# Kernel optimization log

Measured on AMD Instinct MI355X. Metric: run time of the kernel, lower is better.

The kernel has to match this reference:

```python
import jax, jax.numpy as jnp
import numpy as np

N = 50000; E = 800000; H = 4; C = 64; FEAT = 128; EDIM = 16; G = 256
NEG_SLOPE = 0.2; BN_EPS = 1e-5


def _gat_layer(x, src, dst, W, a_src, a_dst, bias, gamma, beta, alpha_edge=None):
    # GATConv (concat=True, PyG math), then BatchNorm1d (batch stats) + ReLU.
    h = (x @ W).reshape(N, H, C)                       # [N,H,C]
    alpha = (h * a_src).sum(-1)[src] + (h * a_dst).sum(-1)[dst]   # [Etot,H]
    if alpha_edge is not None:
        alpha = alpha + alpha_edge
    alpha = jax.nn.leaky_relu(alpha, NEG_SLOPE)
    amax = jax.ops.segment_max(alpha, dst, num_segments=N)        # edge softmax over dst
    ea = jnp.exp(alpha - amax[dst])
    denom = jax.ops.segment_sum(ea, dst, num_segments=N)
    coef = ea / (denom[dst] + 1e-16)
    out = jax.ops.segment_sum(coef[:, :, None] * h[src], dst, num_segments=N)
    out = out.reshape(N, H * C) + bias
    mu = out.mean(0)
    var = out.var(0)
    out = (out - mu) / jnp.sqrt(var + BN_EPS) * gamma + beta
    return jax.nn.relu(out)


def setup_inputs() -> dict:
    key = jax.random.key(0)
    ks = jax.random.split(key, 32)
    s = 0.05
    inp = {
        "x": jax.random.normal(ks[0], (N, FEAT), jnp.float32),
        "edge_index": jax.random.randint(ks[1], (2, E), 0, N),
        "edge_attr": jax.random.normal(ks[2], (E, EDIM), jnp.float32),
        "batch": jnp.sort(jax.random.randint(ks[3], (N,), 0, G)),
    }
    in_dims = [FEAT, H * C, H * C]
    for i in range(3):
        k = 4 + 7 * i
        inp[f"W{i}"] = jax.random.normal(ks[k], (in_dims[i], H * C), jnp.float32) * s
        inp[f"att_src{i}"] = jax.random.normal(ks[k + 1], (H, C), jnp.float32) * s
        inp[f"att_dst{i}"] = jax.random.normal(ks[k + 2], (H, C), jnp.float32) * s
        inp[f"bias{i}"] = jnp.zeros((H * C,), jnp.float32)
        inp[f"gamma{i}"] = jnp.ones((H * C,), jnp.float32)
        inp[f"beta{i}"] = jnp.zeros((H * C,), jnp.float32)
    inp["We0"] = jax.random.normal(ks[28], (EDIM, H * C), jnp.float32) * s
    inp["att_e0"] = jax.random.normal(ks[29], (H, C), jnp.float32) * s
    return inp


def reference(x, edge_index, edge_attr, batch,
              W0, att_src0, att_dst0, bias0, gamma0, beta0,
              W1, att_src1, att_dst1, bias1, gamma1, beta1,
              W2, att_src2, att_dst2, bias2, gamma2, beta2,
              We0, att_e0):
    # PyG GATConv adds self-loops; edge_attr for self-loops filled with mean.
    loops = jnp.arange(N)
    src = jnp.concatenate([edge_index[0], loops])
    dst = jnp.concatenate([edge_index[1], loops])
    ea_sl = jnp.concatenate([edge_attr, jnp.broadcast_to(edge_attr.mean(0), (N, EDIM))], 0)
    e = (ea_sl @ We0).reshape(E + N, H, C)
    alpha_e = (e * att_e0).sum(-1)                     # [Etot,H]
    x = _gat_layer(x, src, dst, W0, att_src0, att_dst0, bias0, gamma0, beta0, alpha_e)
    x = _gat_layer(x, src, dst, W1, att_src1, att_dst1, bias1, gamma1, beta1)
    x = _gat_layer(x, src, dst, W2, att_src2, att_dst2, bias2, gamma2, beta2)
    # global_mean_pool
    counts = jax.ops.segment_sum(jnp.ones((N,), x.dtype), batch, num_segments=G)
    sums = jax.ops.segment_sum(x, batch, num_segments=G)
    return sums / jnp.clip(counts, 1.0)[:, None]
```

## Files before the change

kernel.cpp:

```cpp
#include <hip/hip_runtime.h>
#include <math.h>

#define NN 50000
#define NE 800000
#define ET 850000
#define HCC 256
#define GG 256
#define CAP 64
#define NB 16

constexpr size_t NHC    = (size_t)NN * HCC;
constexpr size_t O_H    = 0;
constexpr size_t O_AGG  = O_H + NHC / 2;
constexpr size_t O_REC  = O_AGG + NHC / 2;
constexpr size_t O_BT0  = O_REC + (size_t)NN * CAP * 4;
constexpr size_t O_BT1  = O_BT0 + 16384;
constexpr size_t O_BT2  = O_BT1 + 32768;
constexpr size_t O_AS   = O_BT2 + 32768;
constexpr size_t O_AD   = O_AS + (size_t)NN * 4;
constexpr size_t O_M    = O_AD + (size_t)NN * 4;
constexpr size_t O_ZERO = O_M + 64;
constexpr size_t O_DEG  = O_ZERO;
constexpr size_t O_SLS  = O_DEG + NN;
constexpr size_t O_PART = O_SLS + 4;
constexpr size_t O_END  = O_PART + 3 * NB * 512;
constexpr size_t ZWORDS = O_END - O_ZERO;
constexpr int    ZBLK   = (int)((ZWORDS / 4 + 255) / 256);

typedef __attribute__((ext_vector_type(8))) short bf16x8;
typedef __attribute__((ext_vector_type(4))) float f32x4;

__device__ inline unsigned short f2bf(float f) {
    unsigned int u = __float_as_uint(f);
    unsigned int r = (u + 0x7fffu + ((u >> 16) & 1u)) >> 16;
    return (unsigned short)r;
}
__device__ inline float b2f(unsigned short u) {
    return __uint_as_float(((unsigned int)u) << 16);
}
__device__ inline float bflo(unsigned int u) { return __uint_as_float(u << 16); }
__device__ inline float bfhi(unsigned int u) { return __uint_as_float(u & 0xffff0000u); }

__global__ void prep_kernel(const float* __restrict__ W0, const float* __restrict__ W1,
                            const float* __restrict__ W2,
                            const float* __restrict__ We0, const float* __restrict__ att_e0,
                            unsigned short* __restrict__ Bt0,
                            unsigned short* __restrict__ Bt1,
                            unsigned short* __restrict__ Bt2,
                            float* __restrict__ M, float* __restrict__ zbase) {
    int b = blockIdx.x;
    if (b >= 641) {
        size_t idx = ((size_t)(b - 641) * 256 + threadIdx.x) * 4;
        if (idx < ZWORDS)
            *(float4*)(zbase + idx) = make_float4(0.f, 0.f, 0.f, 0.f);
        return;
    }
    if (b == 640) {
        int t = threadIdx.x;
        if (t < 64) {
            int k = t >> 2, hh = t & 3;
            float s = 0.f;
            for (int c = 0; c < 64; ++c)
                s += We0[k * 256 + hh * 64 + c] * att_e0[hh * 64 + c];
            M[k * 4 + hh] = s;
        }
        return;
    }
    const float* W; unsigned short* Bt; int K, base;
    if (b < 128)      { W = W0; Bt = Bt0; K = 128; base = 0; }
    else if (b < 384) { W = W1; Bt = Bt1; K = 256; base = 128; }
    else              { W = W2; Bt = Bt2; K = 256; base = 384; }
    int idx = (b - base) * 256 + threadIdx.x;
    int n = idx & 255, k = idx >> 8;
    Bt[(size_t)n * K + k] = f2bf(W[(size_t)k * 256 + n]);
}

__global__ void csr_kernel(const int* __restrict__ srcA, const int* __restrict__ dstA,
                           const float* __restrict__ ea, const float* __restrict__ M,
                           int* __restrict__ deg, uint4* __restrict__ rec,
                           float* __restrict__ slsum) {
    int t0 = blockIdx.x * 2048 + threadIdx.x;
    float a0 = 0.f, a1 = 0.f, a2 = 0.f, a3 = 0.f;
    #pragma unroll
    for (int q = 0; q < 8; ++q) {
        int e = t0 + q * 256;
        if (e < ET) {
            bool real = (e < NE);
            int d = real ? dstA[e] : (e - NE);
            int s = real ? srcA[e] : (e - NE);
            int p = atomicAdd(&deg[d], 1);
            if (p > CAP - 1) p = CAP - 1;
            int slot = d * CAP + p;
            uint4 r;
            r.z = (unsigned)s;
            if (real) {
                r.w = 0u;
                const float4* pp = (const float4*)(ea + (size_t)e * 16);
                float4 va = pp[0], vb = pp[1], vc = pp[2], vd = pp[3];
                float v[16] = {va.x, va.y, va.z, va.w, vb.x, vb.y, vb.z, vb.w,
                               vc.x, vc.y, vc.z, vc.w, vd.x, vd.y, vd.z, vd.w};
                float o0 = 0.f, o1 = 0.f, o2 = 0.f, o3 = 0.f;
                #pragma unroll
                for (int k = 0; k < 16; ++k) {
                    float4 m4 = *(const float4*)(M + k * 4);
                    o0 = fmaf(v[k], m4.x, o0);
                    o1 = fmaf(v[k], m4.y, o1);
                    o2 = fmaf(v[k], m4.z, o2);
                    o3 = fmaf(v[k], m4.w, o3);
                }
                r.x = ((unsigned)f2bf(o1) << 16) | (unsigned)f2bf(o0);
                r.y = ((unsigned)f2bf(o3) << 16) | (unsigned)f2bf(o2);
                a0 += o0; a1 += o1; a2 += o2; a3 += o3;
            } else {
                r.x = 0u; r.y = 0u; r.w = 1u;
            }
            rec[slot] = r;
        }
    }
    #pragma unroll
    for (int off = 32; off; off >>= 1) {
        a0 += __shfl_xor(a0, off);
        a1 += __shfl_xor(a1, off);
        a2 += __shfl_xor(a2, off);
        a3 += __shfl_xor(a3, off);
    }
    __shared__ float part[4][4];
    int wave = threadIdx.x >> 6, lane = threadIdx.x & 63;
    if (lane == 0) {
        part[wave][0] = a0; part[wave][1] = a1;
        part[wave][2] = a2; part[wave][3] = a3;
    }
    __syncthreads();
    if (threadIdx.x < 4)
        atomicAdd(&slsum[threadIdx.x],
                  part[0][threadIdx.x] + part[1][threadIdx.x] +
                  part[2][threadIdx.x] + part[3][threadIdx.x]);
}

template <int K, bool NORM>
__global__ __launch_bounds__(256) void gemm_fused(const float* __restrict__ Af,
                                                  const unsigned short* __restrict__ Ab,
                                                  const unsigned short* __restrict__ Bt,
                                                  const float* __restrict__ part,
                                                  const float* __restrict__ gamma,
                                                  const float* __restrict__ beta,
                                                  const float* __restrict__ att_src,
                                                  const float* __restrict__ att_dst,
                                                  unsigned short* __restrict__ Hout,
                                                  float* __restrict__ asA,
                                                  float* __restrict__ adA, int M) {
    __shared__ unsigned short As[64][40];
    __shared__ unsigned short Bs[256][40];
    __shared__ float kvs[256], cvs[256];
    int tid = threadIdx.x;
    int wave = tid >> 6, lane = tid & 63;
    int quad = lane >> 4, l16 = lane & 15;
    int row0 = blockIdx.x * 64;
    f32x4 acc[4][4] = {};

    if (NORM) {
        int ch = tid;
        float s = 0.f, s2 = 0.f;
        #pragma unroll
        for (int b = 0; b < NB; ++b) {
            s  += part[b * 512 + ch];
            s2 += part[b * 512 + 256 + ch];
        }
        const float invN = 1.0f / (float)NN;
        float mr = s * invN;
        float var = s2 * invN - mr * mr;
        float k = gamma[ch] * rsqrtf(var + 1e-5f);
        kvs[ch] = k;
        cvs[ch] = beta[ch] - mr * k;
        __syncthreads();
    }

    for (int k0 = 0; k0 < K; k0 += 32) {
        {
            int row = tid >> 2, seg = tid & 3;
            ushort4 o0 = make_ushort4(0, 0, 0, 0), o1 = o0;
            if (row0 + row < M) {
                float u[8];
                if (NORM) {
                    uint4 raw = *(const uint4*)(Ab + (size_t)(row0 + row) * K + k0 + seg * 8);
                    u[0] = bflo(raw.x); u[1] = bfhi(raw.x);
                    u[2] = bflo(raw.y); u[3] = bfhi(raw.y);
                    u[4] = bflo(raw.z); u[5] = bfhi(raw.z);
                    u[6] = bflo(raw.w); u[7] = bfhi(raw.w);
                    int cb = k0 + seg * 8;
                    #pragma unroll
                    for (int q = 0; q < 8; ++q)
                        u[q] = fmaxf(fmaf(u[q], kvs[cb + q], cvs[cb + q]), 0.f);
                } else {
                    const float* ap = Af + (size_t)(row0 + row) * K + k0 + seg * 8;
                    float4 f1 = *(const float4*)ap;
                    float4 f2 = *(const float4*)(ap + 4);
                    u[0] = f1.x; u[1] = f1.y; u[2] = f1.z; u[3] = f1.w;
                    u[4] = f2.x; u[5] = f2.y; u[6] = f2.z; u[7] = f2.w;
                }
                o0 = make_ushort4(f2bf(u[0]), f2bf(u[1]), f2bf(u[2]), f2bf(u[3]));
                o1 = make_ushort4(f2bf(u[4]), f2bf(u[5]), f2bf(u[6]), f2bf(u[7]));
            }
            *(ushort4*)&As[row][seg * 8] = o0;
            *(ushort4*)&As[row][seg * 8 + 4] = o1;
        }
        {
            const uint4* src = (const uint4*)(Bt + (size_t)tid * K + k0);
            uint4 b0 = src[0], b1 = src[1], b2 = src[2], b3 = src[3];
            uint4* dst = (uint4*)&Bs[tid][0];
            dst[0] = b0; dst[1] = b1; dst[2] = b2; dst[3] = b3;
        }
        __syncthreads();
        bf16x8 a_frag[4], b_frag[4];
        #pragma unroll
        for (int mi = 0; mi < 4; ++mi)
            a_frag[mi] = *(const bf16x8*)&As[mi * 16 + l16][quad * 8];
        #pragma unroll
        for (int ni = 0; ni < 4; ++ni)
            b_frag[ni] = *(const bf16x8*)&Bs[wave * 64 + ni * 16 + l16][quad * 8];
        #pragma unroll
        for (int mi = 0; mi < 4; ++mi)
            #pragma unroll
            for (int ni = 0; ni < 4; ++ni)
                acc[mi][ni] = __builtin_amdgcn_mfma_f32_16x16x32_bf16(
                    a_frag[mi], b_frag[ni], acc[mi][ni], 0, 0, 0);
        __syncthreads();
    }

    #pragma unroll
    for (int mi = 0; mi < 4; ++mi) {
        #pragma unroll
        for (int reg = 0; reg < 4; ++reg) {
            int r = row0 + mi * 16 + quad * 4 + reg;
            if (r < M) {
                #pragma unroll
                for (int ni = 0; ni < 4; ++ni) {
                    int c = wave * 64 + ni * 16 + l16;
                    Hout[(size_t)r * HCC + c] = f2bf(acc[mi][ni][reg]);
                }
            }
        }
    }
    float asc[4], adc_[4];
    #pragma unroll
    for (int ni = 0; ni < 4; ++ni) {
        asc[ni] = att_src[wave * 64 + ni * 16 + l16];
        adc_[ni] = att_dst[wave * 64 + ni * 16 + l16];
    }
    #pragma unroll
    for (int mi = 0; mi < 4; ++mi) {
        #pragma unroll
        for (int reg = 0; reg < 4; ++reg) {
            float s1 = acc[mi][0][reg] * asc[0] + acc[mi][1][reg] * asc[1] +
                       acc[mi][2][reg] * asc[2] + acc[mi][3][reg] * asc[3];
            float d1 = acc[mi][0][reg] * adc_[0] + acc[mi][1][reg] * adc_[1] +
                       acc[mi][2][reg] * adc_[2] + acc[mi][3][reg] * adc_[3];
            #pragma unroll
            for (int off = 1; off < 16; off <<= 1) {
                s1 += __shfl_xor(s1, off);
                d1 += __shfl_xor(d1, off);
            }
            int r = row0 + mi * 16 + quad * 4 + reg;
            if (l16 == 0 && r < M) {
                asA[(size_t)r * 4 + wave] = s1;
                adA[(size_t)r * 4 + wave] = d1;
            }
        }
    }
}

template <bool HAS_AE>
__global__ __launch_bounds__(512) void agg_kernel(const unsigned short* __restrict__ Hm,
                                                  const float* __restrict__ asA,
                                                  const float* __restrict__ adA,
                                                  const uint4* __restrict__ rec,
                                                  const int* __restrict__ degA,
                                                  const float* __restrict__ slsum,
                                                  unsigned short* __restrict__ outA,
                                                  float* __restrict__ part) {
    __shared__ float wlds[8][260];
    __shared__ float slds[2][8][256];
    int wave = threadIdx.x >> 6, lane = threadIdx.x & 63;
    int n = blockIdx.x * 8 + wave;
    int head = lane >> 4;
    int st = n * CAP;
    int d = degA[n];
    if (d > CAP) d = CAP;
    float4 ad4 = *(const float4*)(adA + (size_t)n * 4);

    float4 w4 = make_float4(0.f, 0.f, 0.f, 0.f);
    int ms = 0;
    if (lane < d) {
        uint4 r = rec[st + lane];
        ms = (int)r.z;
        float4 av = *(const float4*)(asA + (size_t)ms * 4);
        float4 t = make_float4(av.x + ad4.x, av.y + ad4.y, av.z + ad4.z, av.w + ad4.w);
        if (HAS_AE) {
            if (r.w) {
                const float inv = 1.0f / (float)NE;
                t.x += slsum[0] * inv; t.y += slsum[1] * inv;
                t.z += slsum[2] * inv; t.w += slsum[3] * inv;
            } else {
                t.x += bflo(r.x); t.y += bfhi(r.x);
                t.z += bflo(r.y); t.w += bfhi(r.y);
            }
        }
        t.x = (t.x > 0.f) ? t.x : 0.2f * t.x;
        t.y = (t.y > 0.f) ? t.y : 0.2f * t.y;
        t.z = (t.z > 0.f) ? t.z : 0.2f * t.z;
        t.w = (t.w > 0.f) ? t.w : 0.2f * t.w;
        w4.x = __expf(t.x);
        w4.y = __expf(t.y);
        w4.z = __expf(t.z);
        w4.w = __expf(t.w);
    }
    float4 Dv = w4;
    wlds[wave][0 * 65 + lane] = w4.x;
    wlds[wave][1 * 65 + lane] = w4.y;
    wlds[wave][2 * 65 + lane] = w4.z;
    wlds[wave][3 * 65 + lane] = w4.w;

    float4 acc = make_float4(0.f, 0.f, 0.f, 0.f);
    const unsigned short* hb = Hm + lane * 4;
    int cnt8 = (d + 7) & ~7;
    const float* wrow = &wlds[wave][head * 65];

    int sjA[8]; ushort4 hvA[8];
    #pragma unroll
    for (int q = 0; q < 8; ++q)
        sjA[q] = __builtin_amdgcn_readlane(ms, q);
    #pragma unroll
    for (int q = 0; q < 8; ++q)
        hvA[q] = *(const ushort4*)(hb + (size_t)sjA[q] * HCC);
    for (int jj = 0; jj < cnt8; jj += 8) {
        int nj = jj + 8;
        bool more = (nj < cnt8);
        ushort4 hvB[8];
        if (more) {
            int sjB[8];
            #pragma unroll
            for (int q = 0; q < 8; ++q)
                sjB[q] = __builtin_amdgcn_readlane(ms, nj + q);
            #pragma unroll
            for (int q = 0; q < 8; ++q)
                hvB[q] = *(const ushort4*)(hb + (size_t)sjB[q] * HCC);
        }
        float wq[8];
        #pragma unroll
        for (int q = 0; q < 8; ++q)
            wq[q] = wrow[jj + q];
        #pragma unroll
        for (int q = 0; q < 8; ++q) {
            acc.x = fmaf(wq[q], b2f(hvA[q].x), acc.x);
            acc.y = fmaf(wq[q], b2f(hvA[q].y), acc.y);
            acc.z = fmaf(wq[q], b2f(hvA[q].z), acc.z);
            acc.w = fmaf(wq[q], b2f(hvA[q].w), acc.w);
        }
        if (more) {
            #pragma unroll
            for (int q = 0; q < 8; ++q)
                hvA[q] = hvB[q];
        }
    }
    #pragma unroll
    for (int off = 32; off; off >>= 1) {
        Dv.x += __shfl_xor(Dv.x, off);
        Dv.y += __shfl_xor(Dv.y, off);
        Dv.z += __shfl_xor(Dv.z, off);
        Dv.w += __shfl_xor(Dv.w, off);
    }
    float D = (head & 2) ? ((head & 1) ? Dv.w : Dv.z) : ((head & 1) ? Dv.y : Dv.x);
    float inv = 1.0f / (D + 1e-16f);
    float4 o = make_float4(acc.x * inv, acc.y * inv, acc.z * inv, acc.w * inv);
    ushort4 ob = make_ushort4(f2bf(o.x), f2bf(o.y), f2bf(o.z), f2bf(o.w));
    *(ushort4*)(outA + (size_t)n * HCC + lane * 4) = ob;

    *(float4*)&slds[0][wave][lane * 4] = o;
    *(float4*)&slds[1][wave][lane * 4] =
        make_float4(o.x * o.x, o.y * o.y, o.z * o.z, o.w * o.w);
    __syncthreads();
    int t = threadIdx.x;
    if (t < 512) {
        int ch = t & 255, which = t >> 8;
        float s = 0.f;
        #pragma unroll
        for (int w = 0; w < 8; ++w)
            s += slds[which][w][ch];
        int bucket = blockIdx.x & (NB - 1);
        atomicAdd(&part[bucket * 512 + which * 256 + ch], s);
    }
}

__global__ void pool_kernel(const unsigned short* __restrict__ aggb,
                            const float* __restrict__ part,
                            const float* __restrict__ gamma, const float* __restrict__ beta,
                            const int* __restrict__ batch,
                            float* __restrict__ out) {
    int ch = threadIdx.x;
    int g = blockIdx.x;
    float s = 0.f, s2 = 0.f;
    #pragma unroll
    for (int b = 0; b < NB; ++b) {
        s  += part[b * 512 + ch];
        s2 += part[b * 512 + 256 + ch];
    }
    const float invN = 1.0f / (float)NN;
    float mr = s * invN;
    float var = s2 * invN - mr * mr;
    float k = gamma[ch] * rsqrtf(var + 1e-5f);
    float c = beta[ch] - mr * k;

    int lo = 0, hi = NN;
    while (lo < hi) { int mid = (lo + hi) >> 1; if (batch[mid] < g) lo = mid + 1; else hi = mid; }
    int start = lo;
    lo = start; hi = NN;
    while (lo < hi) { int mid = (lo + hi) >> 1; if (batch[mid] < g + 1) lo = mid + 1; else hi = mid; }
    int end = lo;

    float a0 = 0.f, a1 = 0.f, a2 = 0.f, a3 = 0.f;
    int n = start;
    for (; n + 3 < end; n += 4) {
        a0 += fmaxf(fmaf(b2f(aggb[(size_t)n * HCC + ch]), k, c), 0.f);
        a1 += fmaxf(fmaf(b2f(aggb[(size_t)(n + 1) * HCC + ch]), k, c), 0.f);
        a2 += fmaxf(fmaf(b2f(aggb[(size_t)(n + 2) * HCC + ch]), k, c), 0.f);
        a3 += fmaxf(fmaf(b2f(aggb[(size_t)(n + 3) * HCC + ch]), k, c), 0.f);
    }
    for (; n < end; ++n)
        a0 += fmaxf(fmaf(b2f(aggb[(size_t)n * HCC + ch]), k, c), 0.f);
    float tot = (a0 + a1) + (a2 + a3);
    out[(size_t)g * HCC + ch] = tot / fmaxf((float)(end - start), 1.0f);
}

extern "C" void kernel_launch(void* const* d_in, const int* in_sizes, int n_in,
                              void* d_out, int out_size, void* d_ws, size_t ws_size,
                              hipStream_t stream) {
    const float* x = (const float*)d_in[0];
    const int* edge_index = (const int*)d_in[1];
    const int* srcA = edge_index;
    const int* dstA = edge_index + NE;
    const float* edge_attr = (const float*)d_in[2];
    const int* batch = (const int*)d_in[3];
    const float* W[3]   = {(const float*)d_in[4],  (const float*)d_in[10], (const float*)d_in[16]};
    const float* asc[3] = {(const float*)d_in[5],  (const float*)d_in[11], (const float*)d_in[17]};
    const float* adc[3] = {(const float*)d_in[6],  (const float*)d_in[12], (const float*)d_in[18]};
    const float* gam[3] = {(const float*)d_in[8],  (const float*)d_in[14], (const float*)d_in[20]};
    const float* bet[3] = {(const float*)d_in[9],  (const float*)d_in[15], (const float*)d_in[21]};
    const float* We0 = (const float*)d_in[22];
    const float* att_e0 = (const float*)d_in[23];

    float* wsf = (float*)d_ws;
    unsigned short* hbuf = (unsigned short*)(wsf + O_H);
    unsigned short* aggb = (unsigned short*)(wsf + O_AGG);
    uint4* rec   = (uint4*)(wsf + O_REC);
    unsigned short* Bt0  = (unsigned short*)(wsf + O_BT0);
    unsigned short* Bt1  = (unsigned short*)(wsf + O_BT1);
    unsigned short* Bt2  = (unsigned short*)(wsf + O_BT2);
    float* asA   = wsf + O_AS;
    float* adA   = wsf + O_AD;
    float* Mb    = wsf + O_M;
    int*   deg   = (int*)(wsf + O_DEG);
    float* slsum = wsf + O_SLS;
    float* part  = wsf + O_PART;

    prep_kernel<<<641 + ZBLK, 256, 0, stream>>>(W[0], W[1], W[2], We0, att_e0,
                                                Bt0, Bt1, Bt2, Mb, wsf + O_ZERO);
    csr_kernel<<<(ET + 2047) / 2048, 256, 0, stream>>>(srcA, dstA, edge_attr, Mb,
                                                       deg, rec, slsum);

    unsigned short* Bts[3] = {Bt0, Bt1, Bt2};
    for (int L = 0; L < 3; ++L) {
        if (L == 0)
            gemm_fused<128, false><<<782, 256, 0, stream>>>(x, (const unsigned short*)0,
                Bts[0], (const float*)0, gam[0], bet[0], asc[0], adc[0], hbuf, asA, adA, NN);
        else
            gemm_fused<256, true><<<782, 256, 0, stream>>>((const float*)0, aggb,
                Bts[L], part + (size_t)(L - 1) * NB * 512, gam[L - 1], bet[L - 1],
                asc[L], adc[L], hbuf, asA, adA, NN);
        if (L == 0)
            agg_kernel<true><<<6250, 512, 0, stream>>>(hbuf, asA, adA, rec, deg, slsum,
                aggb, part + (size_t)L * NB * 512);
        else
            agg_kernel<false><<<6250, 512, 0, stream>>>(hbuf, asA, adA, rec, deg, slsum,
                aggb, part + (size_t)L * NB * 512);
    }

    pool_kernel<<<GG, 256, 0, stream>>>(aggb, part + (size_t)2 * NB * 512,
                                        gam[2], bet[2], batch, (float*)d_out);
}
```

Measured before the change: 529.7 us.

## Fuse all GAT stages into one persistent cooperative kernel with grid syncs

Replaces the sequence of separate kernel launches (prep, CSR build, three GEMM and aggregation layers, pooling) with a single cooperative persistent kernel that loops over tiles and nodes and separates phases with grid-wide syncs. This removes launch gaps and tail effects between the many small kernels. Per-block BN partial statistics now accumulate across every node a block handles. In exchange, the grid is capped at occupancy-limited block counts with 256-thread blocks instead of 512-thread agg blocks, and the shared-memory union may lower occupancy. The grid syncs themselves also cost time.

```diff
diff --git a/kernel.cpp b/kernel.cpp
--- a/kernel.cpp
+++ b/kernel.cpp
@@ -1,5 +1,8 @@
 #include <hip/hip_runtime.h>
+#include <hip/hip_cooperative_groups.h>
 #include <math.h>
+
+namespace cg = cooperative_groups;
 
 #define NN 50000
 #define NE 800000
@@ -25,7 +28,8 @@
 constexpr size_t O_PART = O_SLS + 4;
 constexpr size_t O_END  = O_PART + 3 * NB * 512;
 constexpr size_t ZWORDS = O_END - O_ZERO;
-constexpr int    ZBLK   = (int)((ZWORDS / 4 + 255) / 256);
+constexpr int    ZJOBS  = (int)((ZWORDS / 4 + 255) / 256);
+constexpr int    NJOBS  = 641 + ZJOBS;
 
 typedef __attribute__((ext_vector_type(8))) short bf16x8;
 typedef __attribute__((ext_vector_type(4))) float f32x4;
@@ -41,121 +45,44 @@
 __device__ inline float bflo(unsigned int u) { return __uint_as_float(u << 16); }
 __device__ inline float bfhi(unsigned int u) { return __uint_as_float(u & 0xffff0000u); }
 
-__global__ void prep_kernel(const float* __restrict__ W0, const float* __restrict__ W1,
-                            const float* __restrict__ W2,
-                            const float* __restrict__ We0, const float* __restrict__ att_e0,
-                            unsigned short* __restrict__ Bt0,
-                            unsigned short* __restrict__ Bt1,
-                            unsigned short* __restrict__ Bt2,
-                            float* __restrict__ M, float* __restrict__ zbase) {
-    int b = blockIdx.x;
-    if (b >= 641) {
-        size_t idx = ((size_t)(b - 641) * 256 + threadIdx.x) * 4;
-        if (idx < ZWORDS)
-            *(float4*)(zbase + idx) = make_float4(0.f, 0.f, 0.f, 0.f);
-        return;
-    }
-    if (b == 640) {
-        int t = threadIdx.x;
-        if (t < 64) {
-            int k = t >> 2, hh = t & 3;
-            float s = 0.f;
-            for (int c = 0; c < 64; ++c)
-                s += We0[k * 256 + hh * 64 + c] * att_e0[hh * 64 + c];
-            M[k * 4 + hh] = s;
-        }
-        return;
-    }
-    const float* W; unsigned short* Bt; int K, base;
-    if (b < 128)      { W = W0; Bt = Bt0; K = 128; base = 0; }
-    else if (b < 384) { W = W1; Bt = Bt1; K = 256; base = 128; }
-    else              { W = W2; Bt = Bt2; K = 256; base = 384; }
-    int idx = (b - base) * 256 + threadIdx.x;
-    int n = idx & 255, k = idx >> 8;
-    Bt[(size_t)n * K + k] = f2bf(W[(size_t)k * 256 + n]);
-}
-
-__global__ void csr_kernel(const int* __restrict__ srcA, const int* __restrict__ dstA,
-                           const float* __restrict__ ea, const float* __restrict__ M,
-                           int* __restrict__ deg, uint4* __restrict__ rec,
-                           float* __restrict__ slsum) {
-    int t0 = blockIdx.x * 2048 + threadIdx.x;
-    float a0 = 0.f, a1 = 0.f, a2 = 0.f, a3 = 0.f;
-    #pragma unroll
-    for (int q = 0; q < 8; ++q) {
-        int e = t0 + q * 256;
-        if (e < ET) {
-            bool real = (e < NE);
-            int d = real ? dstA[e] : (e - NE);
-            int s = real ? srcA[e] : (e - NE);
-            int p = atomicAdd(&deg[d], 1);
-            if (p > CAP - 1) p = CAP - 1;
-            int slot = d * CAP + p;
-            uint4 r;
-            r.z = (unsigned)s;
-            if (real) {
-                r.w = 0u;
-                const float4* pp = (const float4*)(ea + (size_t)e * 16);
-                float4 va = pp[0], vb = pp[1], vc = pp[2], vd = pp[3];
-                float v[16] = {va.x, va.y, va.z, va.w, vb.x, vb.y, vb.z, vb.w,
-                               vc.x, vc.y, vc.z, vc.w, vd.x, vd.y, vd.z, vd.w};
-                float o0 = 0.f, o1 = 0.f, o2 = 0.f, o3 = 0.f;
-                #pragma unroll
-                for (int k = 0; k < 16; ++k) {
-                    float4 m4 = *(const float4*)(M + k * 4);
-                    o0 = fmaf(v[k], m4.x, o0);
-                    o1 = fmaf(v[k], m4.y, o1);
-                    o2 = fmaf(v[k], m4.z, o2);
-                    o3 = fmaf(v[k], m4.w, o3);
-                }
-                r.x = ((unsigned)f2bf(o1) << 16) | (unsigned)f2bf(o0);
-                r.y = ((unsigned)f2bf(o3) << 16) | (unsigned)f2bf(o2);
-                a0 += o0; a1 += o1; a2 += o2; a3 += o3;
-            } else {
-                r.x = 0u; r.y = 0u; r.w = 1u;
-            }
-            rec[slot] = r;
-        }
-    }
-    #pragma unroll
-    for (int off = 32; off; off >>= 1) {
-        a0 += __shfl_xor(a0, off);
-        a1 += __shfl_xor(a1, off);
-        a2 += __shfl_xor(a2, off);
-        a3 += __shfl_xor(a3, off);
-    }
-    __shared__ float part[4][4];
-    int wave = threadIdx.x >> 6, lane = threadIdx.x & 63;
-    if (lane == 0) {
-        part[wave][0] = a0; part[wave][1] = a1;
-        part[wave][2] = a2; part[wave][3] = a3;
-    }
-    __syncthreads();
-    if (threadIdx.x < 4)
-        atomicAdd(&slsum[threadIdx.x],
-                  part[0][threadIdx.x] + part[1][threadIdx.x] +
-                  part[2][threadIdx.x] + part[3][threadIdx.x]);
-}
+union ShMem {
+    struct {
+        unsigned short As[64][40];
+        unsigned short Bs[256][40];
+        float kvs[256];
+        float cvs[256];
+    } g;
+    struct {
+        float wlds[4][260];
+        float slds[2][4][256];
+        float red[4][4];
+    } a;
+};
+
+struct MegaParams {
+    const float* x; const int* srcA; const int* dstA; const float* ea; const int* batch;
+    const float* W0; const float* W1; const float* W2;
+    const float* asc0; const float* adc0; const float* asc1; const float* adc1;
+    const float* asc2; const float* adc2;
+    const float* gam0; const float* bet0; const float* gam1; const float* bet1;
+    const float* gam2; const float* bet2;
+    const float* We0; const float* att_e0;
+    unsigned short* hbuf; unsigned short* aggb; uint4* rec;
+    unsigned short* Bt0; unsigned short* Bt1; unsigned short* Bt2;
+    float* asA; float* adA; float* Mb; int* deg; float* slsum; float* part;
+    float* out;
+};
 
 template <int K, bool NORM>
-__global__ __launch_bounds__(256) void gemm_fused(const float* __restrict__ Af,
-                                                  const unsigned short* __restrict__ Ab,
-                                                  const unsigned short* __restrict__ Bt,
-                                                  const float* __restrict__ part,
-                                                  const float* __restrict__ gamma,
-                                                  const float* __restrict__ beta,
-                                                  const float* __restrict__ att_src,
-                                                  const float* __restrict__ att_dst,
-                                                  unsigned short* __restrict__ Hout,
-                                                  float* __restrict__ asA,
-                                                  float* __restrict__ adA, int M) {
-    __shared__ unsigned short As[64][40];
-    __shared__ unsigned short Bs[256][40];
-    __shared__ float kvs[256], cvs[256];
+__device__ __forceinline__ void dev_gemm(ShMem* sh, int tile,
+        const float* Af, const unsigned short* Ab, const unsigned short* Bt,
+        const float* part, const float* gamma, const float* beta,
+        const float* att_src, const float* att_dst,
+        unsigned short* Hout, float* asA, float* adA) {
     int tid = threadIdx.x;
     int wave = tid >> 6, lane = tid & 63;
     int quad = lane >> 4, l16 = lane & 15;
-    int row0 = blockIdx.x * 64;
+    int row0 = tile * 64;
     f32x4 acc[4][4] = {};
 
     if (NORM) {
@@ -170,8 +97,8 @@
         float mr = s * invN;
         float var = s2 * invN - mr * mr;
         float k = gamma[ch] * rsqrtf(var + 1e-5f);
-        kvs[ch] = k;
-        cvs[ch] = beta[ch] - mr * k;
+        sh->g.kvs[ch] = k;
+        sh->g.cvs[ch] = beta[ch] - mr * k;
         __syncthreads();
     }
 
@@ -179,7 +106,7 @@
         {
             int row = tid >> 2, seg = tid & 3;
             ushort4 o0 = make_ushort4(0, 0, 0, 0), o1 = o0;
-            if (row0 + row < M) {
+            if (row0 + row < NN) {
                 float u[8];
                 if (NORM) {
                     uint4 raw = *(const uint4*)(Ab + (size_t)(row0 + row) * K + k0 + seg * 8);
@@ -190,7 +117,7 @@
                     int cb = k0 + seg * 8;
                     #pragma unroll
                     for (int q = 0; q < 8; ++q)
-                        u[q] = fmaxf(fmaf(u[q], kvs[cb + q], cvs[cb + q]), 0.f);
+                        u[q] = fmaxf(fmaf(u[q], sh->g.kvs[cb + q], sh->g.cvs[cb + q]), 0.f);
                 } else {
                     const float* ap = Af + (size_t)(row0 + row) * K + k0 + seg * 8;
                     float4 f1 = *(const float4*)ap;
@@ -201,23 +128,23 @@
                 o0 = make_ushort4(f2bf(u[0]), f2bf(u[1]), f2bf(u[2]), f2bf(u[3]));
                 o1 = make_ushort4(f2bf(u[4]), f2bf(u[5]), f2bf(u[6]), f2bf(u[7]));
             }
-            *(ushort4*)&As[row][seg * 8] = o0;
-            *(ushort4*)&As[row][seg * 8 + 4] = o1;
+            *(ushort4*)&sh->g.As[row][seg * 8] = o0;
+            *(ushort4*)&sh->g.As[row][seg * 8 + 4] = o1;
         }
         {
             const uint4* src = (const uint4*)(Bt + (size_t)tid * K + k0);
             uint4 b0 = src[0], b1 = src[1], b2 = src[2], b3 = src[3];
-            uint4* dst = (uint4*)&Bs[tid][0];
+            uint4* dst = (uint4*)&sh->g.Bs[tid][0];
             dst[0] = b0; dst[1] = b1; dst[2] = b2; dst[3] = b3;
         }
         __syncthreads();
         bf16x8 a_frag[4], b_frag[4];
         #pragma unroll
         for (int mi = 0; mi < 4; ++mi)
-            a_frag[mi] = *(const bf16x8*)&As[mi * 16 + l16][quad * 8];
+            a_frag[mi] = *(const bf16x8*)&sh->g.As[mi * 16 + l16][quad * 8];
         #pragma unroll
         for (int ni = 0; ni < 4; ++ni)
-            b_frag[ni] = *(const bf16x8*)&Bs[wave * 64 + ni * 16 + l16][quad * 8];
+            b_frag[ni] = *(const bf16x8*)&sh->g.Bs[wave * 64 + ni * 16 + l16][quad * 8];
         #pragma unroll
         for (int mi = 0; mi < 4; ++mi)
             #pragma unroll
@@ -232,7 +159,7 @@
         #pragma unroll
         for (int reg = 0; reg < 4; ++reg) {
             int r = row0 + mi * 16 + quad * 4 + reg;
-            if (r < M) {
+            if (r < NN) {
                 #pragma unroll
                 for (int ni = 0; ni < 4; ++ni) {
                     int c = wave * 64 + ni * 16 + l16;
@@ -261,7 +188,7 @@
                 d1 += __shfl_xor(d1, off);
             }
             int r = row0 + mi * 16 + quad * 4 + reg;
-            if (l16 == 0 && r < M) {
+            if (l16 == 0 && r < NN) {
                 asA[(size_t)r * 4 + wave] = s1;
                 adA[(size_t)r * 4 + wave] = d1;
             }
@@ -270,19 +197,10 @@
 }
 
 template <bool HAS_AE>
-__global__ __launch_bounds__(512) void agg_kernel(const unsigned short* __restrict__ Hm,
-                                                  const float* __restrict__ asA,
-                                                  const float* __restrict__ adA,
-                                                  const uint4* __restrict__ rec,
-                                                  const int* __restrict__ degA,
-                                                  const float* __restrict__ slsum,
-                                                  unsigned short* __restrict__ outA,
-                                                  float* __restrict__ part) {
-    __shared__ float wlds[8][260];
-    __shared__ float slds[2][8][256];
-    int wave = threadIdx.x >> 6, lane = threadIdx.x & 63;
-    int n = blockIdx.x * 8 + wave;
-    int head = lane >> 4;
+__device__ __forceinline__ void dev_agg(float* wldsw, int n, int lane, int head,
+        const unsigned short* Hm, const float* asA, const float* adA,
+        const uint4* rec, const int* degA, const float* slsum,
+        unsigned short* outA, float4& ssum, float4& sssq) {
     int st = n * CAP;
     int d = degA[n];
     if (d > CAP) d = CAP;
@@ -315,35 +233,31 @@
         w4.w = __expf(t.w);
     }
     float4 Dv = w4;
-    wlds[wave][0 * 65 + lane] = w4.x;
-    wlds[wave][1 * 65 + lane] = w4.y;
-    wlds[wave][2 * 65 + lane] = w4.z;
-    wlds[wave][3 * 65 + lane] = w4.w;
+    wldsw[0 * 65 + lane] = w4.x;
+    wldsw[1 * 65 + lane] = w4.y;
+    wldsw[2 * 65 + lane] = w4.z;
+    wldsw[3 * 65 + lane] = w4.w;
 
     float4 acc = make_float4(0.f, 0.f, 0.f, 0.f);
     const unsigned short* hb = Hm + lane * 4;
     int cnt8 = (d + 7) & ~7;
-    const float* wrow = &wlds[wave][head * 65];
-
-    int sjA[8]; ushort4 hvA[8];
+    const float* wrow = &wldsw[head * 65];
+
+    ushort4 hvA[8];
     #pragma unroll
-    for (int q = 0; q < 8; ++q)
-        sjA[q] = __builtin_amdgcn_readlane(ms, q);
-    #pragma unroll
-    for (int q = 0; q < 8; ++q)
-        hvA[q] = *(const ushort4*)(hb + (size_t)sjA[q] * HCC);
+    for (int q = 0; q < 8; ++q) {
+        int sj = __builtin_amdgcn_readlane(ms, q);
+        hvA[q] = *(const ushort4*)(hb + (size_t)sj * HCC);
+    }
     for (int jj = 0; jj < cnt8; jj += 8) {
-        int nj = jj + 8;
-        bool more = (nj < cnt8);
+        bool more = (jj + 8 < cnt8);
         ushort4 hvB[8];
         if (more) {
-            int sjB[8];
             #pragma unroll
-            for (int q = 0; q < 8; ++q)
-                sjB[q] = __builtin_amdgcn_readlane(ms, nj + q);
-            #pragma unroll
-            for (int q = 0; q < 8; ++q)
-                hvB[q] = *(const ushort4*)(hb + (size_t)sjB[q] * HCC);
+            for (int q = 0; q < 8; ++q) {
+                int sj = __builtin_amdgcn_readlane(ms, jj + 8 + q);
+                hvB[q] = *(const ushort4*)(hb + (size_t)sj * HCC);
+            }
         }
         float wq[8];
         #pragma unroll
@@ -374,61 +288,180 @@
     float4 o = make_float4(acc.x * inv, acc.y * inv, acc.z * inv, acc.w * inv);
     ushort4 ob = make_ushort4(f2bf(o.x), f2bf(o.y), f2bf(o.z), f2bf(o.w));
     *(ushort4*)(outA + (size_t)n * HCC + lane * 4) = ob;
-
-    *(float4*)&slds[0][wave][lane * 4] = o;
-    *(float4*)&slds[1][wave][lane * 4] =
-        make_float4(o.x * o.x, o.y * o.y, o.z * o.z, o.w * o.w);
+    ssum.x += o.x; ssum.y += o.y; ssum.z += o.z; ssum.w += o.w;
+    sssq.x = fmaf(o.x, o.x, sssq.x);
+    sssq.y = fmaf(o.y, o.y, sssq.y);
+    sssq.z = fmaf(o.z, o.z, sssq.z);
+    sssq.w = fmaf(o.w, o.w, sssq.w);
+}
+
+template <bool HAS_AE>
+__device__ __forceinline__ void agg_phase(ShMem* sh, const MegaParams& p, float* partL) {
+    int tid = threadIdx.x;
+    int wave = tid >> 6, lane = tid & 63, head = lane >> 4;
+    int totalWaves = gridDim.x * 4;
+    float4 ssum = make_float4(0.f, 0.f, 0.f, 0.f);
+    float4 sssq = make_float4(0.f, 0.f, 0.f, 0.f);
+    for (int n = blockIdx.x * 4 + wave; n < NN; n += totalWaves)
+        dev_agg<HAS_AE>(sh->a.wlds[wave], n, lane, head, p.hbuf, p.asA, p.adA,
+                        p.rec, p.deg, p.slsum, p.aggb, ssum, sssq);
+    *(float4*)&sh->a.slds[0][wave][lane * 4] = ssum;
+    *(float4*)&sh->a.slds[1][wave][lane * 4] = sssq;
     __syncthreads();
-    int t = threadIdx.x;
-    if (t < 512) {
-        int ch = t & 255, which = t >> 8;
-        float s = 0.f;
-        #pragma unroll
-        for (int w = 0; w < 8; ++w)
-            s += slds[which][w][ch];
-        int bucket = blockIdx.x & (NB - 1);
-        atomicAdd(&part[bucket * 512 + which * 256 + ch], s);
-    }
-}
-
-__global__ void pool_kernel(const unsigned short* __restrict__ aggb,
-                            const float* __restrict__ part,
-                            const float* __restrict__ gamma, const float* __restrict__ beta,
-                            const int* __restrict__ batch,
-                            float* __restrict__ out) {
-    int ch = threadIdx.x;
-    int g = blockIdx.x;
-    float s = 0.f, s2 = 0.f;
-    #pragma unroll
-    for (int b = 0; b < NB; ++b) {
-        s  += part[b * 512 + ch];
-        s2 += part[b * 512 + 256 + ch];
-    }
-    const float invN = 1.0f / (float)NN;
-    float mr = s * invN;
-    float var = s2 * invN - mr * mr;
-    float k = gamma[ch] * rsqrtf(var + 1e-5f);
-    float c = beta[ch] - mr * k;
-
-    int lo = 0, hi = NN;
-    while (lo < hi) { int mid = (lo + hi) >> 1; if (batch[mid] < g) lo = mid + 1; else hi = mid; }
-    int start = lo;
-    lo = start; hi = NN;
-    while (lo < hi) { int mid = (lo + hi) >> 1; if (batch[mid] < g + 1) lo = mid + 1; else hi = mid; }
-    int end = lo;
-
-    float a0 = 0.f, a1 = 0.f, a2 = 0.f, a3 = 0.f;
-    int n = start;
-    for (; n + 3 < end; n += 4) {
-        a0 += fmaxf(fmaf(b2f(aggb[(size_t)n * HCC + ch]), k, c), 0.f);
-        a1 += fmaxf(fmaf(b2f(aggb[(size_t)(n + 1) * HCC + ch]), k, c), 0.f);
-        a2 += fmaxf(fmaf(b2f(aggb[(size_t)(n + 2) * HCC + ch]), k, c), 0.f);
-        a3 += fmaxf(fmaf(b2f(aggb[(size_t)(n + 3) * HCC + ch]), k, c), 0.f);
-    }
-    for (; n < end; ++n)
-        a0 += fmaxf(fmaf(b2f(aggb[(size_t)n * HCC + ch]), k, c), 0.f);
-    float tot = (a0 + a1) + (a2 + a3);
-    out[(size_t)g * HCC + ch] = tot / fmaxf((float)(end - start), 1.0f);
+    int ch = tid;
+    float s = sh->a.slds[0][0][ch] + sh->a.slds[0][1][ch] +
+              sh->a.slds[0][2][ch] + sh->a.slds[0][3][ch];
+    float s2 = sh->a.slds[1][0][ch] + sh->a.slds[1][1][ch] +
+               sh->a.slds[1][2][ch] + sh->a.slds[1][3][ch];
+    int bucket = blockIdx.x & (NB - 1);
+    atomicAdd(&partL[bucket * 512 + ch], s);
+    atomicAdd(&partL[bucket * 512 + 256 + ch], s2);
+}
+
+__global__ __launch_bounds__(256, 4) void mega_kernel(MegaParams p) {
+    __shared__ ShMem sh;
+    cg::grid_group grid = cg::this_grid();
+    int tid = threadIdx.x;
+    int wave = tid >> 6, lane = tid & 63;
+
+    for (int job = blockIdx.x; job < NJOBS; job += gridDim.x) {
+        if (job < 640) {
+            const float* W; unsigned short* Bt; int K, base;
+            if (job < 128)      { W = p.W0; Bt = p.Bt0; K = 128; base = 0; }
+            else if (job < 384) { W = p.W1; Bt = p.Bt1; K = 256; base = 128; }
+            else                { W = p.W2; Bt = p.Bt2; K = 256; base = 384; }
+            int idx = (job - base) * 256 + tid;
+            int nn = idx & 255, k = idx >> 8;
+            Bt[(size_t)nn * K + k] = f2bf(W[(size_t)k * 256 + nn]);
+        } else if (job == 640) {
+            if (tid < 64) {
+                int k = tid >> 2, hh = tid & 3;
+                float s = 0.f;
+                for (int c = 0; c < 64; ++c)
+                    s += p.We0[k * 256 + hh * 64 + c] * p.att_e0[hh * 64 + c];
+                p.Mb[k * 4 + hh] = s;
+            }
+        } else {
+            size_t idx = ((size_t)(job - 641) * 256 + tid) * 4;
+            float* zbase = (float*)p.deg;
+            if (idx < ZWORDS)
+                *(float4*)(zbase + idx) = make_float4(0.f, 0.f, 0.f, 0.f);
+        }
+    }
+    grid.sync();
+
+    {
+        float a0 = 0.f, a1 = 0.f, a2 = 0.f, a3 = 0.f;
+        for (int e = blockIdx.x * 256 + tid; e < ET; e += gridDim.x * 256) {
+            bool real = (e < NE);
+            int d = real ? p.dstA[e] : (e - NE);
+            int s = real ? p.srcA[e] : (e - NE);
+            int pp = atomicAdd(&p.deg[d], 1);
+            if (pp > CAP - 1) pp = CAP - 1;
+            int slot = d * CAP + pp;
+            uint4 r;
+            r.z = (unsigned)s;
+            if (real) {
+                r.w = 0u;
+                const float4* q4 = (const float4*)(p.ea + (size_t)e * 16);
+                float4 va = q4[0], vb = q4[1], vc = q4[2], vd = q4[3];
+                float v[16] = {va.x, va.y, va.z, va.w, vb.x, vb.y, vb.z, vb.w,
+                               vc.x, vc.y, vc.z, vc.w, vd.x, vd.y, vd.z, vd.w};
+                float o0 = 0.f, o1 = 0.f, o2 = 0.f, o3 = 0.f;
+                #pragma unroll
+                for (int k = 0; k < 16; ++k) {
+                    float4 m4 = *(const float4*)(p.Mb + k * 4);
+                    o0 = fmaf(v[k], m4.x, o0);
+                    o1 = fmaf(v[k], m4.y, o1);
+                    o2 = fmaf(v[k], m4.z, o2);
+                    o3 = fmaf(v[k], m4.w, o3);
+                }
+                r.x = ((unsigned)f2bf(o1) << 16) | (unsigned)f2bf(o0);
+                r.y = ((unsigned)f2bf(o3) << 16) | (unsigned)f2bf(o2);
+                a0 += o0; a1 += o1; a2 += o2; a3 += o3;
+            } else {
+                r.x = 0u; r.y = 0u; r.w = 1u;
+            }
+            p.rec[slot] = r;
+        }
+        #pragma unroll
+        for (int off = 32; off; off >>= 1) {
+            a0 += __shfl_xor(a0, off);
+            a1 += __shfl_xor(a1, off);
+            a2 += __shfl_xor(a2, off);
+            a3 += __shfl_xor(a3, off);
+        }
+        if (lane == 0) {
+            sh.a.red[wave][0] = a0; sh.a.red[wave][1] = a1;
+            sh.a.red[wave][2] = a2; sh.a.red[wave][3] = a3;
+        }
+        __syncthreads();
+        if (tid < 4)
+            atomicAdd(&p.slsum[tid], sh.a.red[0][tid] + sh.a.red[1][tid] +
+                                     sh.a.red[2][tid] + sh.a.red[3][tid]);
+    }
+    grid.sync();
+
+    for (int tile = blockIdx.x; tile < 782; tile += gridDim.x)
+        dev_gemm<128, false>(&sh, tile, p.x, (const unsigned short*)0, p.Bt0,
+                             (const float*)0, p.gam0, p.bet0, p.asc0, p.adc0,
+                             p.hbuf, p.asA, p.adA);
+    grid.sync();
+    agg_phase<true>(&sh, p, p.part);
+    grid.sync();
+
+    for (int tile = blockIdx.x; tile < 782; tile += gridDim.x)
+        dev_gemm<256, true>(&sh, tile, (const float*)0, p.aggb, p.Bt1,
+                            p.part, p.gam0, p.bet0, p.asc1, p.adc1,
+                            p.hbuf, p.asA, p.adA);
+    grid.sync();
+    agg_phase<false>(&sh, p, p.part + (size_t)NB * 512);
+    grid.sync();
+
+    for (int tile = blockIdx.x; tile < 782; tile += gridDim.x)
+        dev_gemm<256, true>(&sh, tile, (const float*)0, p.aggb, p.Bt2,
+                            p.part + (size_t)NB * 512, p.gam1, p.bet1, p.asc2, p.adc2,
+                            p.hbuf, p.asA, p.adA);
+    grid.sync();
+    agg_phase<false>(&sh, p, p.part + (size_t)2 * NB * 512);
+    grid.sync();
+
+    if (blockIdx.x < GG) {
+        int ch = tid;
+        int g = blockIdx.x;
+        const float* partL = p.part + (size_t)2 * NB * 512;
+        float s = 0.f, s2 = 0.f;
+        #pragma unroll
+        for (int b = 0; b < NB; ++b) {
+            s  += partL[b * 512 + ch];
+            s2 += partL[b * 512 + 256 + ch];
+        }
+        const float invN = 1.0f / (float)NN;
+        float mr = s * invN;
+        float var = s2 * invN - mr * mr;
+        float k = p.gam2[ch] * rsqrtf(var + 1e-5f);
+        float c = p.bet2[ch] - mr * k;
+
+        int lo = 0, hi = NN;
+        while (lo < hi) { int mid = (lo + hi) >> 1; if (p.batch[mid] < g) lo = mid + 1; else hi = mid; }
+        int start = lo;
+        lo = start; hi = NN;
+        while (lo < hi) { int mid = (lo + hi) >> 1; if (p.batch[mid] < g + 1) lo = mid + 1; else hi = mid; }
+        int end = lo;
+
+        float a0 = 0.f, a1 = 0.f, a2 = 0.f, a3 = 0.f;
+        int n = start;
+        for (; n + 3 < end; n += 4) {
+            a0 += fmaxf(fmaf(b2f(p.aggb[(size_t)n * HCC + ch]), k, c), 0.f);
+            a1 += fmaxf(fmaf(b2f(p.aggb[(size_t)(n + 1) * HCC + ch]), k, c), 0.f);
+            a2 += fmaxf(fmaf(b2f(p.aggb[(size_t)(n + 2) * HCC + ch]), k, c), 0.f);
+            a3 += fmaxf(fmaf(b2f(p.aggb[(size_t)(n + 3) * HCC + ch]), k, c), 0.f);
+        }
+        for (; n < end; ++n)
+            a0 += fmaxf(fmaf(b2f(p.aggb[(size_t)n * HCC + ch]), k, c), 0.f);
+        float tot = (a0 + a1) + (a2 + a3);
+        p.out[(size_t)g * HCC + ch] = tot / fmaxf((float)(end - start), 1.0f);
+    }
 }
 
 extern "C" void kernel_launch(void* const* d_in, const int* in_sizes, int n_in,
@@ -436,54 +469,44 @@
                               hipStream_t stream) {
     const float* x = (const float*)d_in[0];
     const int* edge_index = (const int*)d_in[1];
-    const int* srcA = edge_index;
-    const int* dstA = edge_index + NE;
     const float* edge_attr = (const float*)d_in[2];
     const int* batch = (const int*)d_in[3];
-    const float* W[3]   = {(const float*)d_in[4],  (const float*)d_in[10], (const float*)d_in[16]};
-    const float* asc[3] = {(const float*)d_in[5],  (const float*)d_in[11], (const float*)d_in[17]};
-    const float* adc[3] = {(const float*)d_in[6],  (const float*)d_in[12], (const float*)d_in[18]};
-    const float* gam[3] = {(const float*)d_in[8],  (const float*)d_in[14], (const float*)d_in[20]};
-    const float* bet[3] = {(const float*)d_in[9],  (const float*)d_in[15], (const float*)d_in[21]};
-    const float* We0 = (const float*)d_in[22];
-    const float* att_e0 = (const float*)d_in[23];
-
     float* wsf = (float*)d_ws;
-    unsigned short* hbuf = (unsigned short*)(wsf + O_H);
-    unsigned short* aggb = (unsigned short*)(wsf + O_AGG);
-    uint4* rec   = (uint4*)(wsf + O_REC);
-    unsigned short* Bt0  = (unsigned short*)(wsf + O_BT0);
-    unsigned short* Bt1  = (unsigned short*)(wsf + O_BT1);
-    unsigned short* Bt2  = (unsigned short*)(wsf + O_BT2);
-    float* asA   = wsf + O_AS;
-    float* adA   = wsf + O_AD;
-    float* Mb    = wsf + O_M;
-    int*   deg   = (int*)(wsf + O_DEG);
-    float* slsum = wsf + O_SLS;
-    float* part  = wsf + O_PART;
-
-    prep_kernel<<<641 + ZBLK, 256, 0, stream>>>(W[0], W[1], W[2], We0, att_e0,
-                                                Bt0, Bt1, Bt2, Mb, wsf + O_ZERO);
-    csr_kernel<<<(ET + 2047) / 2048, 256, 0, stream>>>(srcA, dstA, edge_attr, Mb,
-                                                       deg, rec, slsum);
-
-    unsigned short* Bts[3] = {Bt0, Bt1, Bt2};
-    for (int L = 0; L < 3; ++L) {
-        if (L == 0)
-            gemm_fused<128, false><<<782, 256, 0, stream>>>(x, (const unsigned short*)0,
-                Bts[0], (const float*)0, gam[0], bet[0], asc[0], adc[0], hbuf, asA, adA, NN);
-        else
-            gemm_fused<256, true><<<782, 256, 0, stream>>>((const float*)0, aggb,
-                Bts[L], part + (size_t)(L - 1) * NB * 512, gam[L - 1], bet[L - 1],
-                asc[L], adc[L], hbuf, asA, adA, NN);
-        if (L == 0)
-            agg_kernel<true><<<6250, 512, 0, stream>>>(hbuf, asA, adA, rec, deg, slsum,
-                aggb, part + (size_t)L * NB * 512);
-        else
-            agg_kernel<false><<<6250, 512, 0, stream>>>(hbuf, asA, adA, rec, deg, slsum,
-                aggb, part + (size_t)L * NB * 512);
-    }
-
-    pool_kernel<<<GG, 256, 0, stream>>>(aggb, part + (size_t)2 * NB * 512,
-                                        gam[2], bet[2], batch, (float*)d_out);
-}
+
+    MegaParams p;
+    p.x = x;
+    p.srcA = edge_index;
+    p.dstA = edge_index + NE;
+    p.ea = edge_attr;
+    p.batch = batch;
+    p.W0 = (const float*)d_in[4];  p.W1 = (const float*)d_in[10]; p.W2 = (const float*)d_in[16];
+    p.asc0 = (const float*)d_in[5];  p.adc0 = (const float*)d_in[6];
+    p.asc1 = (const float*)d_in[11]; p.adc1 = (const float*)d_in[12];
+    p.asc2 = (const float*)d_in[17]; p.adc2 = (const float*)d_in[18];
+    p.gam0 = (const float*)d_in[8];  p.bet0 = (const float*)d_in[9];
+    p.gam1 = (const float*)d_in[14]; p.bet1 = (const float*)d_in[15];
+    p.gam2 = (const float*)d_in[20]; p.bet2 = (const float*)d_in[21];
+    p.We0 = (const float*)d_in[22];
+    p.att_e0 = (const float*)d_in[23];
+    p.hbuf = (unsigned short*)(wsf + O_H);
+    p.aggb = (unsigned short*)(wsf + O_AGG);
+    p.rec  = (uint4*)(wsf + O_REC);
+    p.Bt0  = (unsigned short*)(wsf + O_BT0);
+    p.Bt1  = (unsigned short*)(wsf + O_BT1);
+    p.Bt2  = (unsigned short*)(wsf + O_BT2);
+    p.asA  = wsf + O_AS;
+    p.adA  = wsf + O_AD;
+    p.Mb   = wsf + O_M;
+    p.deg  = (int*)(wsf + O_DEG);
+    p.slsum= wsf + O_SLS;
+    p.part = wsf + O_PART;
+    p.out  = (float*)d_out;
+
+    int per = 0;
+    hipOccupancyMaxActiveBlocksPerMultiprocessor(&per, mega_kernel, 256, 0);
+    if (per < 1) per = 1;
+    if (per > 8) per = 8;
+    dim3 grid(per * 256), block(256);
+    void* args[] = { (void*)&p };
+    hipLaunchCooperativeKernel((const void*)mega_kernel, grid, block, args, 0, stream);
+}
```

After: 1.221 ms. +130.4%, slower.
